# Optimization experiments

Hardware: AMD Instinct MI355X
Metric: run time of the kernel (lower is better)

Reference implementation:

```python
import jax, jax.numpy as jnp
import numpy as np

TEMPERATURE = 0.1

def setup_inputs() -> dict:
    key = jax.random.key(0)
    ks = jax.random.split(key, 6)
    B, K, D, H, N = 256, 32, 128, 256, 16
    z = jax.random.normal(ks[0], (B, K, D), dtype=jnp.float32)
    # edge MLP params: Linear(2D->H), GELU, Linear(H->D)
    W1 = jax.random.normal(ks[1], (2 * D, H), dtype=jnp.float32) * (1.0 / np.sqrt(2 * D))
    b1 = jnp.zeros((H,), dtype=jnp.float32)
    W2 = jax.random.normal(ks[2], (H, D), dtype=jnp.float32) * (1.0 / np.sqrt(H))
    b2 = jnp.zeros((D,), dtype=jnp.float32)
    codebook = jax.random.normal(ks[3], (N, D), dtype=jnp.float32) * 0.02
    return {"z": z, "W1": W1, "b1": b1, "W2": W2, "b2": b2, "codebook": codebook}

def reference(z, W1, b1, W2, b2, codebook):
    # z: (B,K,D). Edge MLP on concat([z_i, z_j]) == split-weight GEMMs,
    # avoiding materializing the (B,K,K,2D) concat tensor.
    D = z.shape[-1]
    h_i = jnp.einsum('bkd,dh->bkh', z, W1[:D])   # contribution of z_i
    h_j = jnp.einsum('bkd,dh->bkh', z, W1[D:])   # contribution of z_j
    h = h_i[:, :, None, :] + h_j[:, None, :, :] + b1       # (B,K,K,H)
    h = jax.nn.gelu(h, approximate=False)                    # torch nn.GELU default = exact erf
    e_ij = jnp.einsum('bijh,hd->bijd', h, W2) + b2           # (B,K,K,D)
    logits = jnp.einsum('bijd,nd->bijn', e_ij, codebook) / TEMPERATURE  # (B,K,K,N)
    alpha_ij = jax.nn.softmax(logits, axis=-1)
    m_ij = jnp.einsum('bijn,nd->bijd', alpha_ij, codebook)   # (B,K,K,D)
    return (m_ij, alpha_ij, e_ij, logits)
```

## Files before the change

kernel.cpp:

```cpp
#include <hip/hip_runtime.h>
#include <hip/hip_bf16.h>
#include <math.h>

#define BB 256
#define KK 32
#define DD 128
#define HH 256
#define NN 16
#define O0 ((size_t)0)
#define O1 ((size_t)33554432)
#define O2 ((size_t)37748736)
#define O3 ((size_t)71303168)

typedef float f32x4 __attribute__((ext_vector_type(4)));
typedef short s16x8 __attribute__((ext_vector_type(8)));

static __device__ __forceinline__ short f2bf(float x) {
  __hip_bfloat16 h = __float2bfloat16(x);
  return *reinterpret_cast<short*>(&h);
}
static __device__ __forceinline__ float bf2f(short s) {
  __hip_bfloat16 h;
  *reinterpret_cast<short*>(&h) = s;
  return __bfloat162float(h);
}
static __device__ __forceinline__ unsigned cvt_pk_bf16(float a, float b) {
  unsigned r;
  asm volatile("v_cvt_pk_bf16_f32 %0, %1, %2" : "=v"(r) : "v"(a), "v"(b));
  return r;
}

static __device__ __forceinline__ float gelu_exact(float x) {
  float ax = fabsf(x) * 0.70710678118654752f;
  float t = __builtin_amdgcn_rcpf(fmaf(0.3275911f, ax, 1.0f));
  float p = fmaf(1.061405429f, t, -1.453152027f);
  p = fmaf(p, t, 1.421413741f);
  p = fmaf(p, t, -0.284496736f);
  p = fmaf(p, t, 0.254829592f);
  p *= t;
  float e = __expf(-ax * ax);
  float er = fmaf(-p, e, 1.0f);
  er = copysignf(er, x);
  return 0.5f * x * (1.0f + er);
}

__global__ __launch_bounds__(256) void prep_kernel(
    const float* __restrict__ z, const float* __restrict__ W1,
    const float* __restrict__ W2, const float* __restrict__ cb,
    const float* __restrict__ b2,
    short* __restrict__ zb, short* __restrict__ W1th, short* __restrict__ W1tl,
    short* __restrict__ Wh, short* __restrict__ Wl, short* __restrict__ cbT,
    short* __restrict__ Vh, short* __restrict__ Vl, float* __restrict__ b2cb) {
  const int idx = blockIdx.x * 256 + threadIdx.x;
  zb[idx] = f2bf(z[idx]);
  if (idx < 512 * 128) {
    int c = idx >> 7, k = idx & 127;
    float w = (c < 256) ? W1[(size_t)k * 256 + c]
                        : W1[(size_t)(128 + k) * 256 + (c - 256)];
    short h = f2bf(w);
    W1th[idx] = h;
    W1tl[idx] = f2bf(w - bf2f(h));
  }
  if (idx < 128 * 256) {
    int c = idx >> 8, k = idx & 255;
    float w = W2[(size_t)k * 128 + c];
    short h = f2bf(w);
    Wh[idx] = h;
    Wl[idx] = f2bf(w - bf2f(h));
  }
  if (idx < 128 * 32) {
    int c = idx >> 5, n = idx & 31;
    cbT[idx] = (n < 16) ? f2bf(cb[(size_t)n * 128 + c]) : (short)0;
  }
  if (idx < 16 * 256) {
    int n = idx >> 8, k = idx & 255;
    float s = 0.f;
#pragma unroll 4
    for (int c = 0; c < 128; ++c)
      s += W2[(size_t)k * 128 + c] * cb[(size_t)n * 128 + c];
    short h = f2bf(s);
    Vh[idx] = h;
    Vl[idx] = f2bf(s - bf2f(h));
  }
  if (idx < 16) {
    float s = 0.f;
    for (int c = 0; c < 128; ++c) s += b2[c] * cb[(size_t)idx * 128 + c];
    b2cb[idx] = s;
  }
}

__global__ __launch_bounds__(256) void hproj_mfma(
    const short* __restrict__ zb, const short* __restrict__ W1th,
    const short* __restrict__ W1tl, const float* __restrict__ b1,
    float* __restrict__ H) {
  const int tid = threadIdx.x;
  const int lane = tid & 63;
  const int wv = tid >> 6;
  const int l4 = lane >> 4, l15 = lane & 15;
  const int row0 = blockIdx.x * 32;
  const int col0 = blockIdx.y * 128 + wv * 32;

  f32x4 acc[2][2];
#pragma unroll
  for (int mt = 0; mt < 2; ++mt)
#pragma unroll
    for (int nt = 0; nt < 2; ++nt)
      acc[mt][nt] = (f32x4){0.f, 0.f, 0.f, 0.f};

#pragma unroll
  for (int ks = 0; ks < 4; ++ks) {
    const int kof = ks * 32 + l4 * 8;
    s16x8 a0 = *(const s16x8*)(zb + (size_t)(row0 + l15) * 128 + kof);
    s16x8 a1 = *(const s16x8*)(zb + (size_t)(row0 + 16 + l15) * 128 + kof);
    s16x8 bh0 = *(const s16x8*)(W1th + (size_t)(col0 + l15) * 128 + kof);
    s16x8 bh1 = *(const s16x8*)(W1th + (size_t)(col0 + 16 + l15) * 128 + kof);
    s16x8 bl0 = *(const s16x8*)(W1tl + (size_t)(col0 + l15) * 128 + kof);
    s16x8 bl1 = *(const s16x8*)(W1tl + (size_t)(col0 + 16 + l15) * 128 + kof);
    acc[0][0] = __builtin_amdgcn_mfma_f32_16x16x32_bf16(a0, bh0, acc[0][0], 0, 0, 0);
    acc[0][0] = __builtin_amdgcn_mfma_f32_16x16x32_bf16(a0, bl0, acc[0][0], 0, 0, 0);
    acc[0][1] = __builtin_amdgcn_mfma_f32_16x16x32_bf16(a0, bh1, acc[0][1], 0, 0, 0);
    acc[0][1] = __builtin_amdgcn_mfma_f32_16x16x32_bf16(a0, bl1, acc[0][1], 0, 0, 0);
    acc[1][0] = __builtin_amdgcn_mfma_f32_16x16x32_bf16(a1, bh0, acc[1][0], 0, 0, 0);
    acc[1][0] = __builtin_amdgcn_mfma_f32_16x16x32_bf16(a1, bl0, acc[1][0], 0, 0, 0);
    acc[1][1] = __builtin_amdgcn_mfma_f32_16x16x32_bf16(a1, bh1, acc[1][1], 0, 0, 0);
    acc[1][1] = __builtin_amdgcn_mfma_f32_16x16x32_bf16(a1, bl1, acc[1][1], 0, 0, 0);
  }

#pragma unroll
  for (int nt = 0; nt < 2; ++nt) {
    const int col = col0 + nt * 16 + l15;
    const float bias = (col0 < 256) ? b1[col] : 0.f;
#pragma unroll
    for (int mt = 0; mt < 2; ++mt)
#pragma unroll
      for (int r = 0; r < 4; ++r)
        H[(size_t)(row0 + mt * 16 + l4 * 4 + r) * 512 + col] =
            acc[mt][nt][r] + bias;
  }
}

#define MFMA16(d, a, bsrc) d = __builtin_amdgcn_mfma_f32_16x16x32_bf16(a, bsrc, d, 0, 0, 0)

__global__ __launch_bounds__(256, 4) void pair_kernel(
    const float* __restrict__ Hcat, const short* __restrict__ Wh,
    const short* __restrict__ Wl, const float* __restrict__ b2,
    const short* __restrict__ Vh, const short* __restrict__ Vl,
    const float* __restrict__ b2cb, const short* __restrict__ cbT,
    float* __restrict__ out) {
  __shared__ short sAh[32 * 256];
  __shared__ short sAl[32 * 256];
  __shared__ short sAlp[32 * 32];

  const int tid = threadIdx.x;
  const int d = blockIdx.x;
  const int blk = (d & 7) * 1024 + (d >> 3);
  const int b = blk >> 5;

  ((unsigned*)sAlp)[tid] = 0u;
  ((unsigned*)sAlp)[tid + 256] = 0u;

  {
    const int k0 = (tid & 127) * 2;
    const int pb = (tid >> 7) * 16;
    const float2 hiv = *(const float2*)(Hcat + (size_t)blk * 512 + k0);
    const float hx = hiv.x;
    const float hy = hiv.y;
    const float* hjp = Hcat + ((size_t)b * KK + pb) * 512 + 256 + k0;
    unsigned* aH = (unsigned*)sAh;
    unsigned* aL = (unsigned*)sAl;
    const int cw = tid & 127;
#pragma unroll 4
    for (int p = 0; p < 16; ++p) {
      const int row = pb + p;
      float2 hj = *(const float2*)(hjp + (size_t)p * 512);
      float g0 = gelu_exact(hx + hj.x);
      float g1 = gelu_exact(hy + hj.y);
      unsigned h01 = cvt_pk_bf16(g0, g1);
      float h0f = __uint_as_float(h01 << 16);
      float h1f = __uint_as_float(h01 & 0xFFFF0000u);
      unsigned l01 = cvt_pk_bf16(g0 - h0f, g1 - h1f);
      const int wi = row * 128 + ((cw ^ ((row & 7) << 2)));
      aH[wi] = h01;
      aL[wi] = l01;
    }
  }
  __syncthreads();

  const int lane = tid & 63;
  const int wv = tid >> 6;
  const int nb = wv * 32;
  const int l4 = lane >> 4;
  const int l15 = lane & 15;
  const bool lw = (wv < 2);

  f32x4 eacc[2][2];
#pragma unroll
  for (int w = 0; w < 2; ++w)
#pragma unroll
    for (int a = 0; a < 2; ++a)
      eacc[w][a] = (f32x4){0.f, 0.f, 0.f, 0.f};
  f32x4 lacc = (f32x4){0.f, 0.f, 0.f, 0.f};

  const int sw = (l15 & 7) << 4;
  const char* pAh = (const char*)sAh;
  const char* pAl = (const char*)sAl;
  const size_t gB0 = (size_t)(nb + l15) * 256 + l4 * 8;
  const size_t gV0 = (size_t)l15 * 256 + l4 * 8;

#pragma unroll
  for (int ks = 0; ks < 8; ++ks) {
    const int cbyte = ks * 64 + l4 * 16;
    const int o0 = l15 * 512 + (cbyte ^ sw);
    const int o1 = (16 + l15) * 512 + (cbyte ^ sw);
    s16x8 ah0 = *(const s16x8*)(pAh + o0);
    s16x8 ah1 = *(const s16x8*)(pAh + o1);
    s16x8 al0 = *(const s16x8*)(pAl + o0);
    s16x8 al1 = *(const s16x8*)(pAl + o1);
    const size_t g0 = gB0 + ks * 32;
    const size_t g1 = g0 + 16 * 256;
    s16x8 bh0 = *(const s16x8*)(Wh + g0);
    s16x8 bh1 = *(const s16x8*)(Wh + g1);
    s16x8 bl0 = *(const s16x8*)(Wl + g0);
    s16x8 bl1 = *(const s16x8*)(Wl + g1);

    MFMA16(eacc[0][0], bh0, ah0); MFMA16(eacc[0][0], bh0, al0);
    MFMA16(eacc[0][0], bl0, ah0);
    MFMA16(eacc[0][1], bh0, ah1); MFMA16(eacc[0][1], bh0, al1);
    MFMA16(eacc[0][1], bl0, ah1);
    MFMA16(eacc[1][0], bh1, ah0); MFMA16(eacc[1][0], bh1, al0);
    MFMA16(eacc[1][0], bl1, ah0);
    MFMA16(eacc[1][1], bh1, ah1); MFMA16(eacc[1][1], bh1, al1);
    MFMA16(eacc[1][1], bl1, ah1);

    if (lw) {
      s16x8 vh = *(const s16x8*)(Vh + gV0 + ks * 32);
      s16x8 vl = *(const s16x8*)(Vl + gV0 + ks * 32);
      s16x8 aF = (wv == 1) ? ah1 : ah0;
      s16x8 aG = (wv == 1) ? al1 : al0;
      MFMA16(lacc, aF, vh);
      MFMA16(lacc, aG, vh);
      MFMA16(lacc, aF, vl);
    }
  }

  {
    const float4 b2q0 = *(const float4*)(b2 + nb + l4 * 4);
    const float4 b2q1 = *(const float4*)(b2 + nb + 16 + l4 * 4);
    float* eg = out + O2 + (size_t)blk * (KK * DD);
#pragma unroll
    for (int a = 0; a < 2; ++a) {
      const int row = a * 16 + l15;
      float4 v0 = make_float4(eacc[0][a][0] + b2q0.x, eacc[0][a][1] + b2q0.y,
                              eacc[0][a][2] + b2q0.z, eacc[0][a][3] + b2q0.w);
      float4 v1 = make_float4(eacc[1][a][0] + b2q1.x, eacc[1][a][1] + b2q1.y,
                              eacc[1][a][2] + b2q1.z, eacc[1][a][3] + b2q1.w);
      *(float4*)(eg + row * 128 + nb + l4 * 4) = v0;
      *(float4*)(eg + row * 128 + nb + 16 + l4 * 4) = v1;
    }
  }

  {
    const float b2cbv = b2cb[l15];
    if (lw) {
      float* lg_out = out + O3 + (size_t)blk * (KK * NN);
      float* ag_out = out + O1 + (size_t)blk * (KK * NN);
#pragma unroll
      for (int r = 0; r < 4; ++r) {
        const int row = wv * 16 + l4 * 4 + r;
        float lg = (lacc[r] + b2cbv) * 10.0f;
        float mx = lg;
#pragma unroll
        for (int m = 1; m < 16; m <<= 1) mx = fmaxf(mx, __shfl_xor(mx, m));
        float p = __expf(lg - mx);
        float s = p;
#pragma unroll
        for (int m = 1; m < 16; m <<= 1) s += __shfl_xor(s, m);
        float a = p / s;
        lg_out[row * 16 + l15] = lg;
        ag_out[row * 16 + l15] = a;
        sAlp[row * 32 + l15] = f2bf(a);
      }
    }
  }
  __syncthreads();

  {
    float* mg = out + O0 + (size_t)blk * (KK * DD);
#pragma unroll
    for (int rg = 0; rg < 2; ++rg) {
      s16x8 af = *(const s16x8*)(sAlp + (rg * 16 + l15) * 32 + l4 * 8);
#pragma unroll
      for (int nt = 0; nt < 2; ++nt) {
        const int c = nb + nt * 16 + l15;
        s16x8 bf = *(const s16x8*)(cbT + (size_t)c * 32 + l4 * 8);
        f32x4 mac = (f32x4){0.f, 0.f, 0.f, 0.f};
        MFMA16(mac, af, bf);
#pragma unroll
        for (int r = 0; r < 4; ++r)
          mg[(rg * 16 + l4 * 4 + r) * 128 + c] = mac[r];
      }
    }
  }
}

extern "C" void kernel_launch(void* const* d_in, const int* in_sizes, int n_in,
                              void* d_out, int out_size, void* d_ws, size_t ws_size,
                              hipStream_t stream) {
  const float* z  = (const float*)d_in[0];
  const float* W1 = (const float*)d_in[1];
  const float* b1 = (const float*)d_in[2];
  const float* W2 = (const float*)d_in[3];
  const float* b2 = (const float*)d_in[4];
  const float* cb = (const float*)d_in[5];
  float* out = (float*)d_out;

  float* Hcat = (float*)d_ws;
  short* zb   = (short*)(Hcat + (size_t)8192 * 512);
  short* W1th = zb + (size_t)1048576;
  short* W1tl = W1th + (size_t)65536;
  short* Wh   = W1tl + (size_t)65536;
  short* Wl   = Wh + (size_t)32768;
  short* cbT  = Wl + (size_t)32768;
  short* Vh   = cbT + (size_t)4096;
  short* Vl   = Vh + (size_t)4096;
  float* b2cb = (float*)(Vl + (size_t)4096);

  prep_kernel<<<4096, 256, 0, stream>>>(z, W1, W2, cb, b2, zb, W1th, W1tl, Wh,
                                        Wl, cbT, Vh, Vl, b2cb);
  hproj_mfma<<<dim3(256, 4), 256, 0, stream>>>(zb, W1th, W1tl, b1, Hcat);
  pair_kernel<<<BB * KK, 256, 0, stream>>>(Hcat, Wh, Wl, b2, Vh, Vl, b2cb,
                                           cbT, out);
}
```

Measured before the change: 232.3 us.

## Keep GELU tiles in registers and split pair work by j-rows per wave

The pair kernel now uses 128-thread blocks where each wave owns 16 j-rows and computes all 128 output columns. The GELU-activated hidden values are built directly in MFMA operand registers instead of being staged through a 32KB shared-memory tile, which removes the block-wide barriers and most LDS traffic. Each wave now also does its own logits/softmax and codebook MFMA, so the idle half of the waves in that stage goes away. In exchange, every wave streams the full W2 hi/lo weights from global/L2 and register pressure rises, with 8 accumulators and 16 A fragments held live.

Result: slower. 355.1 us (+52.9%).

```diff
diff --git a/kernel.cpp b/kernel.cpp
--- a/kernel.cpp
+++ b/kernel.cpp
@@ -28,6 +28,12 @@
   unsigned r;
   asm volatile("v_cvt_pk_bf16_f32 %0, %1, %2" : "=v"(r) : "v"(a), "v"(b));
   return r;
+}
+static __device__ __forceinline__ float bflo(unsigned h) {
+  return __uint_as_float(h << 16);
+}
+static __device__ __forceinline__ float bfhi(unsigned h) {
+  return __uint_as_float(h & 0xFFFF0000u);
 }
 
 static __device__ __forceinline__ float gelu_exact(float x) {
@@ -141,164 +147,126 @@
 
 #define MFMA16(d, a, bsrc) d = __builtin_amdgcn_mfma_f32_16x16x32_bf16(a, bsrc, d, 0, 0, 0)
 
-__global__ __launch_bounds__(256, 4) void pair_kernel(
+__global__ __launch_bounds__(128, 3) void pair_kernel(
     const float* __restrict__ Hcat, const short* __restrict__ Wh,
     const short* __restrict__ Wl, const float* __restrict__ b2,
     const short* __restrict__ Vh, const short* __restrict__ Vl,
     const float* __restrict__ b2cb, const short* __restrict__ cbT,
     float* __restrict__ out) {
-  __shared__ short sAh[32 * 256];
-  __shared__ short sAl[32 * 256];
-  __shared__ short sAlp[32 * 32];
+  __shared__ short alpT[2][16 * 32];
 
   const int tid = threadIdx.x;
-  const int d = blockIdx.x;
-  const int blk = (d & 7) * 1024 + (d >> 3);
+  const int wv = tid >> 6;
+  const int lane = tid & 63;
+  const int l4 = lane >> 4, l15 = lane & 15;
+  const int dd = blockIdx.x;
+  const int blk = (dd & 7) * 1024 + (dd >> 3);
   const int b = blk >> 5;
-
-  ((unsigned*)sAlp)[tid] = 0u;
-  ((unsigned*)sAlp)[tid + 256] = 0u;
-
+  const int j0 = wv * 16;
+
+  *(uint4*)((char*)&alpT[wv][0] + lane * 16) = make_uint4(0u, 0u, 0u, 0u);
+
+  s16x8 Ah[8], Al[8];
   {
-    const int k0 = (tid & 127) * 2;
-    const int pb = (tid >> 7) * 16;
-    const float2 hiv = *(const float2*)(Hcat + (size_t)blk * 512 + k0);
-    const float hx = hiv.x;
-    const float hy = hiv.y;
-    const float* hjp = Hcat + ((size_t)b * KK + pb) * 512 + 256 + k0;
-    unsigned* aH = (unsigned*)sAh;
-    unsigned* aL = (unsigned*)sAl;
-    const int cw = tid & 127;
-#pragma unroll 4
-    for (int p = 0; p < 16; ++p) {
-      const int row = pb + p;
-      float2 hj = *(const float2*)(hjp + (size_t)p * 512);
-      float g0 = gelu_exact(hx + hj.x);
-      float g1 = gelu_exact(hy + hj.y);
-      unsigned h01 = cvt_pk_bf16(g0, g1);
-      float h0f = __uint_as_float(h01 << 16);
-      float h1f = __uint_as_float(h01 & 0xFFFF0000u);
-      unsigned l01 = cvt_pk_bf16(g0 - h0f, g1 - h1f);
-      const int wi = row * 128 + ((cw ^ ((row & 7) << 2)));
-      aH[wi] = h01;
-      aL[wi] = l01;
-    }
-  }
-  __syncthreads();
-
-  const int lane = tid & 63;
-  const int wv = tid >> 6;
-  const int nb = wv * 32;
-  const int l4 = lane >> 4;
-  const int l15 = lane & 15;
-  const bool lw = (wv < 2);
-
-  f32x4 eacc[2][2];
-#pragma unroll
-  for (int w = 0; w < 2; ++w)
-#pragma unroll
-    for (int a = 0; a < 2; ++a)
-      eacc[w][a] = (f32x4){0.f, 0.f, 0.f, 0.f};
+    const float* hib = Hcat + (size_t)blk * 512;
+    const float* hjb = Hcat + ((size_t)(b * KK + j0 + l15)) * 512 + 256;
+#pragma unroll
+    for (int ks = 0; ks < 8; ++ks) {
+      const int k = ks * 32 + l4 * 8;
+      float4 hi0 = *(const float4*)(hib + k);
+      float4 hi1 = *(const float4*)(hib + k + 4);
+      float4 hj0 = *(const float4*)(hjb + k);
+      float4 hj1 = *(const float4*)(hjb + k + 4);
+      float g0 = gelu_exact(hi0.x + hj0.x);
+      float g1 = gelu_exact(hi0.y + hj0.y);
+      float g2 = gelu_exact(hi0.z + hj0.z);
+      float g3 = gelu_exact(hi0.w + hj0.w);
+      float g4 = gelu_exact(hi1.x + hj1.x);
+      float g5 = gelu_exact(hi1.y + hj1.y);
+      float g6 = gelu_exact(hi1.z + hj1.z);
+      float g7 = gelu_exact(hi1.w + hj1.w);
+      unsigned h0 = cvt_pk_bf16(g0, g1);
+      unsigned h1 = cvt_pk_bf16(g2, g3);
+      unsigned h2 = cvt_pk_bf16(g4, g5);
+      unsigned h3 = cvt_pk_bf16(g6, g7);
+      unsigned q0 = cvt_pk_bf16(g0 - bflo(h0), g1 - bfhi(h0));
+      unsigned q1 = cvt_pk_bf16(g2 - bflo(h1), g3 - bfhi(h1));
+      unsigned q2 = cvt_pk_bf16(g4 - bflo(h2), g5 - bfhi(h2));
+      unsigned q3 = cvt_pk_bf16(g6 - bflo(h3), g7 - bfhi(h3));
+      unsigned hv[4] = {h0, h1, h2, h3};
+      unsigned lv[4] = {q0, q1, q2, q3};
+      Ah[ks] = *(const s16x8*)hv;
+      Al[ks] = *(const s16x8*)lv;
+    }
+  }
+
+  f32x4 eacc[8];
+#pragma unroll
+  for (int nt = 0; nt < 8; ++nt) eacc[nt] = (f32x4){0.f, 0.f, 0.f, 0.f};
   f32x4 lacc = (f32x4){0.f, 0.f, 0.f, 0.f};
 
-  const int sw = (l15 & 7) << 4;
-  const char* pAh = (const char*)sAh;
-  const char* pAl = (const char*)sAl;
-  const size_t gB0 = (size_t)(nb + l15) * 256 + l4 * 8;
-  const size_t gV0 = (size_t)l15 * 256 + l4 * 8;
-
+  const size_t wk0 = (size_t)l15 * 256 + l4 * 8;
 #pragma unroll
   for (int ks = 0; ks < 8; ++ks) {
-    const int cbyte = ks * 64 + l4 * 16;
-    const int o0 = l15 * 512 + (cbyte ^ sw);
-    const int o1 = (16 + l15) * 512 + (cbyte ^ sw);
-    s16x8 ah0 = *(const s16x8*)(pAh + o0);
-    s16x8 ah1 = *(const s16x8*)(pAh + o1);
-    s16x8 al0 = *(const s16x8*)(pAl + o0);
-    s16x8 al1 = *(const s16x8*)(pAl + o1);
-    const size_t g0 = gB0 + ks * 32;
-    const size_t g1 = g0 + 16 * 256;
-    s16x8 bh0 = *(const s16x8*)(Wh + g0);
-    s16x8 bh1 = *(const s16x8*)(Wh + g1);
-    s16x8 bl0 = *(const s16x8*)(Wl + g0);
-    s16x8 bl1 = *(const s16x8*)(Wl + g1);
-
-    MFMA16(eacc[0][0], bh0, ah0); MFMA16(eacc[0][0], bh0, al0);
-    MFMA16(eacc[0][0], bl0, ah0);
-    MFMA16(eacc[0][1], bh0, ah1); MFMA16(eacc[0][1], bh0, al1);
-    MFMA16(eacc[0][1], bl0, ah1);
-    MFMA16(eacc[1][0], bh1, ah0); MFMA16(eacc[1][0], bh1, al0);
-    MFMA16(eacc[1][0], bl1, ah0);
-    MFMA16(eacc[1][1], bh1, ah1); MFMA16(eacc[1][1], bh1, al1);
-    MFMA16(eacc[1][1], bl1, ah1);
-
-    if (lw) {
-      s16x8 vh = *(const s16x8*)(Vh + gV0 + ks * 32);
-      s16x8 vl = *(const s16x8*)(Vl + gV0 + ks * 32);
-      s16x8 aF = (wv == 1) ? ah1 : ah0;
-      s16x8 aG = (wv == 1) ? al1 : al0;
-      MFMA16(lacc, aF, vh);
-      MFMA16(lacc, aG, vh);
-      MFMA16(lacc, aF, vl);
+    const int ko = ks * 32;
+    s16x8 vh = *(const s16x8*)(Vh + wk0 + ko);
+    s16x8 vl = *(const s16x8*)(Vl + wk0 + ko);
+    MFMA16(lacc, Ah[ks], vh);
+    MFMA16(lacc, Al[ks], vh);
+    MFMA16(lacc, Ah[ks], vl);
+#pragma unroll
+    for (int nt = 0; nt < 8; ++nt) {
+      const size_t g = (size_t)(nt * 16) * 256 + wk0 + ko;
+      s16x8 wh = *(const s16x8*)(Wh + g);
+      s16x8 wl = *(const s16x8*)(Wl + g);
+      MFMA16(eacc[nt], wh, Ah[ks]);
+      MFMA16(eacc[nt], wh, Al[ks]);
+      MFMA16(eacc[nt], wl, Ah[ks]);
     }
   }
 
   {
-    const float4 b2q0 = *(const float4*)(b2 + nb + l4 * 4);
-    const float4 b2q1 = *(const float4*)(b2 + nb + 16 + l4 * 4);
-    float* eg = out + O2 + (size_t)blk * (KK * DD);
-#pragma unroll
-    for (int a = 0; a < 2; ++a) {
-      const int row = a * 16 + l15;
-      float4 v0 = make_float4(eacc[0][a][0] + b2q0.x, eacc[0][a][1] + b2q0.y,
-                              eacc[0][a][2] + b2q0.z, eacc[0][a][3] + b2q0.w);
-      float4 v1 = make_float4(eacc[1][a][0] + b2q1.x, eacc[1][a][1] + b2q1.y,
-                              eacc[1][a][2] + b2q1.z, eacc[1][a][3] + b2q1.w);
-      *(float4*)(eg + row * 128 + nb + l4 * 4) = v0;
-      *(float4*)(eg + row * 128 + nb + 16 + l4 * 4) = v1;
+    float* eg = out + O2 + (size_t)blk * (KK * DD) + (size_t)(j0 + l15) * DD;
+#pragma unroll
+    for (int nt = 0; nt < 8; ++nt) {
+      const float4 bq = *(const float4*)(b2 + nt * 16 + l4 * 4);
+      float4 v = make_float4(eacc[nt][0] + bq.x, eacc[nt][1] + bq.y,
+                             eacc[nt][2] + bq.z, eacc[nt][3] + bq.w);
+      *(float4*)(eg + nt * 16 + l4 * 4) = v;
     }
   }
 
   {
-    const float b2cbv = b2cb[l15];
-    if (lw) {
-      float* lg_out = out + O3 + (size_t)blk * (KK * NN);
-      float* ag_out = out + O1 + (size_t)blk * (KK * NN);
-#pragma unroll
-      for (int r = 0; r < 4; ++r) {
-        const int row = wv * 16 + l4 * 4 + r;
-        float lg = (lacc[r] + b2cbv) * 10.0f;
-        float mx = lg;
-#pragma unroll
-        for (int m = 1; m < 16; m <<= 1) mx = fmaxf(mx, __shfl_xor(mx, m));
-        float p = __expf(lg - mx);
-        float s = p;
-#pragma unroll
-        for (int m = 1; m < 16; m <<= 1) s += __shfl_xor(s, m);
-        float a = p / s;
-        lg_out[row * 16 + l15] = lg;
-        ag_out[row * 16 + l15] = a;
-        sAlp[row * 32 + l15] = f2bf(a);
-      }
-    }
-  }
-  __syncthreads();
+    const float bcv = b2cb[l15];
+    float* lg_out = out + O3 + (size_t)blk * (KK * NN);
+    float* ag_out = out + O1 + (size_t)blk * (KK * NN);
+#pragma unroll
+    for (int r = 0; r < 4; ++r) {
+      const int row = j0 + l4 * 4 + r;
+      float lg = (lacc[r] + bcv) * 10.0f;
+      float mx = lg;
+#pragma unroll
+      for (int m = 1; m < 16; m <<= 1) mx = fmaxf(mx, __shfl_xor(mx, m));
+      float p = __expf(lg - mx);
+      float s = p;
+#pragma unroll
+      for (int m = 1; m < 16; m <<= 1) s += __shfl_xor(s, m);
+      float a = p / s;
+      lg_out[row * 16 + l15] = lg;
+      ag_out[row * 16 + l15] = a;
+      alpT[wv][(l4 * 4 + r) * 32 + l15] = f2bf(a);
+    }
+  }
 
   {
-    float* mg = out + O0 + (size_t)blk * (KK * DD);
-#pragma unroll
-    for (int rg = 0; rg < 2; ++rg) {
-      s16x8 af = *(const s16x8*)(sAlp + (rg * 16 + l15) * 32 + l4 * 8);
-#pragma unroll
-      for (int nt = 0; nt < 2; ++nt) {
-        const int c = nb + nt * 16 + l15;
-        s16x8 bf = *(const s16x8*)(cbT + (size_t)c * 32 + l4 * 8);
-        f32x4 mac = (f32x4){0.f, 0.f, 0.f, 0.f};
-        MFMA16(mac, af, bf);
-#pragma unroll
-        for (int r = 0; r < 4; ++r)
-          mg[(rg * 16 + l4 * 4 + r) * 128 + c] = mac[r];
-      }
+    s16x8 af = *(const s16x8*)(&alpT[wv][l15 * 32 + l4 * 8]);
+    float* mg = out + O0 + (size_t)blk * (KK * DD) + (size_t)(j0 + l15) * DD;
+#pragma unroll
+    for (int nt = 0; nt < 8; ++nt) {
+      s16x8 cf = *(const s16x8*)(cbT + (size_t)(nt * 16 + l15) * 32 + l4 * 8);
+      f32x4 mac = (f32x4){0.f, 0.f, 0.f, 0.f};
+      MFMA16(mac, cf, af);
+      *(float4*)(mg + nt * 16 + l4 * 4) = *(float4*)&mac;
     }
   }
 }
@@ -328,6 +296,6 @@
   prep_kernel<<<4096, 256, 0, stream>>>(z, W1, W2, cb, b2, zb, W1th, W1tl, Wh,
                                         Wl, cbT, Vh, Vl, b2cb);
   hproj_mfma<<<dim3(256, 4), 256, 0, stream>>>(zb, W1th, W1tl, b1, Hcat);
-  pair_kernel<<<BB * KK, 256, 0, stream>>>(Hcat, Wh, Wl, b2, Vh, Vl, b2cb,
+  pair_kernel<<<BB * KK, 128, 0, stream>>>(Hcat, Wh, Wl, b2, Vh, Vl, b2cb,
                                            cbT, out);
 }
```
